# Optimization experiments

Measured on AMD Instinct MI355X. Metric: run time of the kernel, lower is better.

Reference implementation:

```python
import jax, jax.numpy as jnp
import numpy as np

DIM = 512
N_HEADS = 8
N_KV_HEADS = 4
HEAD_DIM = DIM // N_HEADS  # 64
N_REP = N_HEADS // N_KV_HEADS  # 2
THETA = 10000.0
EPS_RMS = 1e-6
EPS_Z = 1e-6


def setup_inputs() -> dict:
    key = jax.random.key(0)
    ks = jax.random.split(key, 6)
    s = 1.0 / np.sqrt(DIM)
    return {
        "x": jax.random.normal(ks[0], (4, 8192, DIM), dtype=jnp.float32),
        "norm_w": jnp.ones((DIM,), dtype=jnp.float32),
        "wq": jax.random.normal(ks[1], (DIM, DIM), dtype=jnp.float32) * s,
        "wk": jax.random.normal(ks[2], (N_KV_HEADS * HEAD_DIM, DIM), dtype=jnp.float32) * s,
        "wv": jax.random.normal(ks[3], (N_KV_HEADS * HEAD_DIM, DIM), dtype=jnp.float32) * s,
        "wo": jax.random.normal(ks[4], (DIM, DIM), dtype=jnp.float32) * s,
    }


def _rope_cos_sin(seq_len, head_dim):
    # freqs_cis = polar(1, t * theta^(-2i/d))
    inv = 1.0 / (THETA ** (jnp.arange(0, head_dim, 2, dtype=jnp.float32) / head_dim))
    ang = jnp.arange(seq_len, dtype=jnp.float32)[:, None] * inv[None, :]  # (S, d/2)
    return jnp.cos(ang), jnp.sin(ang)


def _apply_rope(t, cos, sin):
    # t: (B, S, H, d); complex rotation on consecutive pairs
    B, S, H, d = t.shape
    tr = t.reshape(B, S, H, d // 2, 2)
    xr, xi = tr[..., 0], tr[..., 1]
    c = cos[None, :, None, :]  # (1, S, 1, d/2)
    s = sin[None, :, None, :]
    out = jnp.stack([xr * c - xi * s, xr * s + xi * c], axis=-1)
    return out.reshape(B, S, H, d)


def _forward(x, norm_w, wq, wk, wv, wo):
    B, S, _ = x.shape
    # RMSNorm
    x = x * jax.lax.rsqrt(jnp.mean(x * x, axis=-1, keepdims=True) + EPS_RMS) * norm_w
    xq = (x @ wq.T).reshape(B, S, N_HEADS, HEAD_DIM)
    xk = (x @ wk.T).reshape(B, S, N_KV_HEADS, HEAD_DIM)
    xv = (x @ wv.T).reshape(B, S, N_KV_HEADS, HEAD_DIM)
    cos, sin = _rope_cos_sin(S, HEAD_DIM)
    xq = _apply_rope(xq, cos, sin)
    xk = _apply_rope(xk, cos, sin)
    # repeat_kv: (B,S,Hkv,d) -> (B,S,Hkv*n_rep,d)
    keys = jnp.repeat(xk, N_REP, axis=2)
    values = jnp.repeat(xv, N_REP, axis=2)
    # to (B, H, S, d)
    Q = jnp.transpose(xq, (0, 2, 1, 3))
    K = jnp.transpose(keys, (0, 2, 1, 3))
    V = jnp.transpose(values, (0, 2, 1, 3))
    phi = lambda t: jax.nn.elu(t) + 1.0
    Q_lin, K_lin = phi(Q), phi(K)
    # Faithful to source: elementwise product reduced over s -> (B,H,d)
    KV = jnp.einsum('bhsd,bhsd->bhd', K_lin, V)
    K_sum = K_lin.sum(axis=2)  # (B,H,d)
    Z = jnp.einsum('bhsd,bhd->bhs', Q_lin, K_sum)[..., None]  # (B,H,S,1)
    Y = Q_lin * KV[:, :, None, :] / (Z + EPS_Z)  # (B,H,S,d)
    Y = jnp.transpose(Y, (0, 2, 1, 3)).reshape(B, S, N_HEADS * HEAD_DIM)
    return Y @ wo.T


def reference(x, norm_w, wq, wk, wv, wo):
    return _forward(x, norm_w, wq, wk, wv, wo)
```

## Files before the change

kernel.cpp:

```cpp
#include <hip/hip_runtime.h>
#include <cmath>

typedef __attribute__((ext_vector_type(8))) short short8;
typedef __attribute__((ext_vector_type(4))) float floatx4;

#define T_TOK 32768
#define DIMK 512
#define AKT 2097152

__device__ __forceinline__ unsigned short f2bf(float f) {
  union { float f; unsigned int u; } v; v.f = f;
  unsigned int r = (v.u + 0x7fffu + ((v.u >> 16) & 1u)) >> 16;
  return (unsigned short)r;
}
__device__ __forceinline__ float bf2f(unsigned short h) {
  union { unsigned int u; float f; } v; v.u = ((unsigned int)h) << 16;
  return v.f;
}

__device__ __forceinline__ void gload_lds16(const unsigned short* g, unsigned short* ldsbase) {
  __builtin_amdgcn_global_load_lds(
      (const __attribute__((address_space(1))) unsigned int*)g,
      (__attribute__((address_space(3))) unsigned int*)ldsbase, 16, 0, 0);
}

__global__ __launch_bounds__(256) void k_prep(const float* __restrict__ x,
    const float* __restrict__ norm_w, const float* __restrict__ wq,
    const float* __restrict__ wk, const float* __restrict__ wv,
    const float* __restrict__ wo, unsigned short* __restrict__ Wb,
    unsigned short* __restrict__ wob, float2* __restrict__ rope,
    float* __restrict__ KVz, unsigned short* __restrict__ xn) {
  if (blockIdx.x < 2048) {
    int i = blockIdx.x * 256 + threadIdx.x;
    int R = i >> 9, col = i & 511;
    float v;
    if (i < 262144) {
      v = wq[i];
    } else {
      int h = (R - 512) >> 7, rem = (R - 512) & 127;
      if (rem < 64) v = wk[(h * 64 + rem) * 512 + col];
      else          v = wv[(h * 64 + rem - 64) * 512 + col];
    }
    Wb[(col >> 6) * 65536 + R * 64 + (col & 63)] = f2bf(v);
    if (i < 262144) {
      wob[(col >> 6) * 32768 + R * 64 + (col & 63)] = f2bf(wo[i]);
      int s = i >> 5, m = i & 31;
      const double c0 = 0.74989420933245582;
      double c1 = c0 * c0, c2 = c1 * c1, c3 = c2 * c2, c4 = c3 * c3;
      double p = 1.0;
      if (m & 1)  p *= c0;
      if (m & 2)  p *= c1;
      if (m & 4)  p *= c2;
      if (m & 8)  p *= c3;
      if (m & 16) p *= c4;
      double ang = (double)s * p;
      const double TWO_PI = 6.2831853071795864769;
      double q = rint(ang * (1.0 / TWO_PI));
      double r = fma(-q, TWO_PI, ang);
      float rf = (float)r;
      rope[i] = make_float2(cosf(rf), sinf(rf));
    }
    if (i < 2048) KVz[i] = 0.f;
  } else {
    int bid = blockIdx.x - 2048;
    int wave = threadIdx.x >> 6, lane = threadIdx.x & 63;
    size_t t = (size_t)bid * 4 + wave;
    const float4* xr = (const float4*)(x + t * DIMK);
    float4 a = xr[lane * 2];
    float4 b = xr[lane * 2 + 1];
    float ss = a.x * a.x + a.y * a.y + a.z * a.z + a.w * a.w
             + b.x * b.x + b.y * b.y + b.z * b.z + b.w * b.w;
    #pragma unroll
    for (int off = 32; off >= 1; off >>= 1) ss += __shfl_xor(ss, off, 64);
    float scale = rsqrtf(ss * (1.0f / DIMK) + 1e-6f);
    const float4* wr = (const float4*)norm_w;
    float4 w0 = wr[lane * 2], w1 = wr[lane * 2 + 1];
    uint4 o;
    o.x = (unsigned int)f2bf(a.x * scale * w0.x) | ((unsigned int)f2bf(a.y * scale * w0.y) << 16);
    o.y = (unsigned int)f2bf(a.z * scale * w0.z) | ((unsigned int)f2bf(a.w * scale * w0.w) << 16);
    o.z = (unsigned int)f2bf(b.x * scale * w1.x) | ((unsigned int)f2bf(b.y * scale * w1.y) << 16);
    o.w = (unsigned int)f2bf(b.z * scale * w1.z) | ((unsigned int)f2bf(b.w * scale * w1.w) << 16);
    *(uint4*)(xn + (size_t)(lane >> 3) * AKT + t * 64 + (lane & 7) * 8) = o;
  }
}

template <bool BF16_OUT, bool FUSE>
__global__ __launch_bounds__(512, 2) void k_gemm256(const unsigned short* __restrict__ A,
    const unsigned short* __restrict__ Bw, void* __restrict__ Cv, int ldc, int nrows,
    const float2* __restrict__ rope, float* __restrict__ KV, float* __restrict__ Ksum) {
  extern __shared__ __align__(16) unsigned short smem[];
  unsigned short* const AsP = smem;
  unsigned short* const BsP = smem + 32768;

  const int tid = threadIdx.x;
  const int wave = tid >> 6, lane = tid & 63;
  const int r = lane & 15, quad = lane >> 4, r7 = r & 7;
  const int wm = (wave >> 2) * 128, wn = (wave & 3) * 64;

  const int ngy = gridDim.y;
  const int bid = blockIdx.x + gridDim.x * blockIdx.y;
  const int xcd = bid & 7;
  const int j = bid >> 3;
  const int lg = (ngy == 4) ? 2 : 1;
  const int per = (gridDim.x * ngy) >> (3 + lg);
  const int mt = xcd * per + (j >> lg);
  const int nt = j & (ngy - 1);
  const int m0 = mt * 256, n0 = nt * 256;

  const int srow = lane >> 3;
  const int scb = (lane & 7) ^ srow;
  const size_t bkt = (size_t)nrows * 64;
  const unsigned short* const Asrc = A + (size_t)(m0 + wave * 8 + srow) * 64 + scb * 8;
  const unsigned short* const Bsrc = Bw + (size_t)(n0 + wave * 8 + srow) * 64 + scb * 8;
  unsigned short* const Adst = AsP + wave * 8 * 64;
  unsigned short* const Bdst = BsP + wave * 8 * 64;

#define STAGE_A(buf, h, kt) do { \
    gload_lds16(Asrc + (size_t)(kt) * AKT + (h) * 8192, Adst + (buf) * 16384 + ((h) * 128) * 64); \
    gload_lds16(Asrc + (size_t)(kt) * AKT + (h) * 8192 + 4096, Adst + (buf) * 16384 + ((h) * 128 + 64) * 64); \
  } while (0)
#define STAGE_B(buf, h, kt) do { \
    gload_lds16(Bsrc + (size_t)(kt) * bkt + (h) * 8192, Bdst + (buf) * 16384 + ((h) * 128) * 64); \
    gload_lds16(Bsrc + (size_t)(kt) * bkt + (h) * 8192 + 4096, Bdst + (buf) * 16384 + ((h) * 128 + 64) * 64); \
  } while (0)

  short8 af[4][2], b0[2][2], b1[2][2];
  floatx4 acc[8][4];
  #pragma unroll
  for (int i = 0; i < 8; i++)
    #pragma unroll
    for (int jj = 0; jj < 4; jj++)
      acc[i][jj] = (floatx4){0.f, 0.f, 0.f, 0.f};

#define LDA8(buf, ah) do { \
    _Pragma("unroll") for (int ii = 0; ii < 4; ii++) \
      _Pragma("unroll") for (int kk = 0; kk < 2; kk++) \
        af[ii][kk] = *(const short8*)&AsP[(buf) * 16384 + (wm + (ah) * 64 + ii * 16 + r) * 64 + ((kk * 4 + quad) ^ r7) * 8]; \
  } while (0)
#define LDB4(buf, bh, arr) do { \
    _Pragma("unroll") for (int jj = 0; jj < 2; jj++) \
      _Pragma("unroll") for (int kk = 0; kk < 2; kk++) \
        arr[jj][kk] = *(const short8*)&BsP[(buf) * 16384 + (wn + (bh) * 32 + jj * 16 + r) * 64 + ((kk * 4 + quad) ^ r7) * 8]; \
  } while (0)
#define MFMAQ(ah, bh, arr) do { \
    __builtin_amdgcn_s_setprio(1); \
    _Pragma("unroll") for (int ii = 0; ii < 4; ii++) \
      _Pragma("unroll") for (int jj = 0; jj < 2; jj++) \
        _Pragma("unroll") for (int kk = 0; kk < 2; kk++) \
          acc[(ah) * 4 + ii][(bh) * 2 + jj] = __builtin_amdgcn_mfma_f32_16x16x32_bf16( \
              af[ii][kk], arr[jj][kk], acc[(ah) * 4 + ii][(bh) * 2 + jj], 0, 0, 0); \
    __builtin_amdgcn_s_setprio(0); \
  } while (0)
#define BAR() do { asm volatile("" ::: "memory"); __builtin_amdgcn_s_barrier(); asm volatile("" ::: "memory"); } while (0)
#define VMW(n) do { asm volatile("s_waitcnt vmcnt(" #n ")" ::: "memory"); __builtin_amdgcn_sched_barrier(0); } while (0)

  STAGE_A(0, 0, 0); STAGE_B(0, 0, 0); STAGE_A(0, 1, 0); STAGE_B(0, 1, 0);
  STAGE_A(1, 0, 1); STAGE_B(1, 0, 1); STAGE_A(1, 1, 1); STAGE_B(1, 1, 1);
  VMW(8);
  BAR();

  #pragma unroll
  for (int it = 0; it < 3; ++it) {
    const int kt = it * 2;
    LDA8(0, 0); LDB4(0, 0, b0);
    BAR(); MFMAQ(0, 0, b0); BAR();
    LDB4(0, 1, b1);
    BAR(); MFMAQ(0, 1, b1); BAR();
    LDA8(0, 1); STAGE_B(0, 0, kt + 2); STAGE_B(0, 1, kt + 2);
    BAR(); MFMAQ(1, 1, b1); BAR();
    STAGE_A(0, 0, kt + 2); STAGE_A(0, 1, kt + 2);
    BAR(); MFMAQ(1, 0, b0); VMW(8); BAR();
    LDA8(1, 0); LDB4(1, 0, b0);
    BAR(); MFMAQ(0, 0, b0); BAR();
    LDB4(1, 1, b1);
    BAR(); MFMAQ(0, 1, b1); BAR();
    LDA8(1, 1); STAGE_B(1, 0, kt + 3); STAGE_B(1, 1, kt + 3);
    BAR(); MFMAQ(1, 1, b1); BAR();
    STAGE_A(1, 0, kt + 3); STAGE_A(1, 1, kt + 3);
    BAR(); MFMAQ(1, 0, b0); VMW(8); BAR();
  }

  LDA8(0, 0); LDB4(0, 0, b0);
  BAR(); MFMAQ(0, 0, b0); BAR();
  LDB4(0, 1, b1);
  BAR(); MFMAQ(0, 1, b1); BAR();
  LDA8(0, 1);
  BAR(); MFMAQ(1, 1, b1); BAR();
  MFMAQ(1, 0, b0); VMW(0); BAR();
  LDA8(1, 0); LDB4(1, 0, b0);
  BAR(); MFMAQ(0, 0, b0); BAR();
  LDB4(1, 1, b1);
  BAR(); MFMAQ(0, 1, b1); BAR();
  LDA8(1, 1);
  BAR(); MFMAQ(1, 1, b1); BAR();
  MFMAQ(1, 0, b0);

  if (FUSE && n0 >= 512) {
#define VSW(t, d) ((t) * 128 + ((d) & 15) + (((((d) >> 4) + ((t) >> 2)) & 7) << 4))
    const int b = m0 >> 13;
    const int kh = ((n0 - 512) >> 8) * 2 + (wn >> 7);
    const int hvb = (wn >> 7) << 6;
    float* const Vs = (float*)smem;
    __syncthreads();
    if (wn & 64) {
      #pragma unroll
      for (int i = 0; i < 8; i++)
        #pragma unroll
        for (int j2 = 0; j2 < 4; j2++)
          #pragma unroll
          for (int p = 0; p < 4; p++) {
            int t = wm + i * 16 + quad * 4 + p;
            Vs[VSW(t, hvb + j2 * 16 + r)] = acc[i][j2][p];
          }
    }
    __syncthreads();
    if (!(wn & 64)) {
      float kvp[4] = {0.f, 0.f, 0.f, 0.f};
      float ksp[4] = {0.f, 0.f, 0.f, 0.f};
      #pragma unroll
      for (int i = 0; i < 8; i++)
        #pragma unroll
        for (int p = 0; p < 4; p++) {
          int t = wm + i * 16 + quad * 4 + p;
          int pos = (m0 + t) & 8191;
          #pragma unroll
          for (int j2 = 0; j2 < 4; j2++) {
            float v = acc[i][j2][p];
            float vp = __shfl_xor(v, 1, 64);
            int d = j2 * 16 + r;
            float2 cs = rope[pos * 32 + (d >> 1)];
            float rk = (r & 1) ? (vp * cs.y + v * cs.x) : (v * cs.x - vp * cs.y);
            rk = rk > 0.f ? rk + 1.f : __expf(rk);
            kvp[j2] += rk * Vs[VSW(t, hvb + d)];
            ksp[j2] += rk;
          }
        }
      #pragma unroll
      for (int j2 = 0; j2 < 4; j2++) {
        kvp[j2] += __shfl_xor(kvp[j2], 16, 64); kvp[j2] += __shfl_xor(kvp[j2], 32, 64);
        ksp[j2] += __shfl_xor(ksp[j2], 16, 64); ksp[j2] += __shfl_xor(ksp[j2], 32, 64);
      }
      if (lane < 16) {
        int base = (b * 4 + kh) * 64 + r;
        #pragma unroll
        for (int j2 = 0; j2 < 4; j2++) {
          atomicAdd(&KV[base + j2 * 16], kvp[j2]);
          atomicAdd(&Ksum[base + j2 * 16], ksp[j2]);
        }
      }
    }
#undef VSW
  } else {
    #pragma unroll
    for (int i = 0; i < 8; i++)
      #pragma unroll
      for (int j2 = 0; j2 < 4; j2++) {
        int row = m0 + wm + i * 16 + quad * 4;
        int col = n0 + wn + j2 * 16 + r;
        #pragma unroll
        for (int p = 0; p < 4; p++) {
          if constexpr (BF16_OUT) {
            ((unsigned short*)Cv)[(size_t)(row + p) * ldc + col] = f2bf(acc[i][j2][p]);
          } else {
            ((float*)Cv)[(size_t)(row + p) * ldc + col] = acc[i][j2][p];
          }
        }
      }
  }
#undef STAGE_A
#undef STAGE_B
#undef LDA8
#undef LDB4
#undef MFMAQ
#undef BAR
#undef VMW
}

__global__ __launch_bounds__(256) void k_qkern(const unsigned short* __restrict__ qkv,
    const float2* __restrict__ rope, const float* __restrict__ KV,
    const float* __restrict__ Ksum, unsigned short* __restrict__ Yb) {
  const int h = threadIdx.x >> 5;
  const int pr = threadIdx.x & 31;
  for (int t = blockIdx.x; t < T_TOK; t += gridDim.x) {
    int b = t >> 13, pos = t & 8191;
    unsigned int qp = *(const unsigned int*)(qkv + (size_t)t * 512 + h * 64 + 2 * pr);
    float qx = bf2f((unsigned short)(qp & 0xffffu));
    float qy = bf2f((unsigned short)(qp >> 16));
    float2 cs = rope[pos * 32 + pr];
    float ar = qx * cs.x - qy * cs.y;
    float ai = qx * cs.y + qy * cs.x;
    ar = ar > 0.f ? ar + 1.f : __expf(ar);
    ai = ai > 0.f ? ai + 1.f : __expf(ai);
    int bk = b * 4 + (h >> 1);
    float2 ks = *(const float2*)(Ksum + bk * 64 + 2 * pr);
    float z = ar * ks.x + ai * ks.y;
    #pragma unroll
    for (int off = 16; off >= 1; off >>= 1) z += __shfl_xor(z, off, 64);
    float2 kv = *(const float2*)(KV + bk * 64 + 2 * pr);
    float inv = 1.0f / (z + 1e-6f);
    unsigned int o = (unsigned int)f2bf(ar * kv.x * inv)
                   | ((unsigned int)f2bf(ai * kv.y * inv) << 16);
    *(unsigned int*)(Yb + (size_t)h * AKT + t * 64 + 2 * pr) = o;
  }
}

extern "C" void kernel_launch(void* const* d_in, const int* in_sizes, int n_in,
                              void* d_out, int out_size, void* d_ws, size_t ws_size,
                              hipStream_t stream) {
  const float* x = (const float*)d_in[0];
  const float* norm_w = (const float*)d_in[1];
  const float* wq = (const float*)d_in[2];
  const float* wk = (const float*)d_in[3];
  const float* wv = (const float*)d_in[4];
  const float* wo = (const float*)d_in[5];
  float* out = (float*)d_out;

  char* ws = (char*)d_ws;
  unsigned short* xn  = (unsigned short*)(ws);
  unsigned short* Wb  = (unsigned short*)(ws + 33554432);
  unsigned short* wob = (unsigned short*)(ws + 34603008);
  unsigned short* qkv = (unsigned short*)(ws + 35127296);
  float2* rope        = (float2*)(ws + 102236160);
  float* KV           = (float*)(ws + 104333312);
  float* Ksum         = (float*)(ws + 104337408);
  unsigned short* Yb  = (unsigned short*)(ws + 104341504);

  static bool s_attr = false;
  if (!s_attr) {
    (void)hipFuncSetAttribute(reinterpret_cast<const void*>(&k_gemm256<true, true>),
                              hipFuncAttributeMaxDynamicSharedMemorySize, 131072);
    (void)hipFuncSetAttribute(reinterpret_cast<const void*>(&k_gemm256<false, false>),
                              hipFuncAttributeMaxDynamicSharedMemorySize, 131072);
    s_attr = true;
  }

  k_prep<<<10240, 256, 0, stream>>>(x, norm_w, wq, wk, wv, wo, Wb, wob, rope, KV, xn);
  k_gemm256<true, true><<<dim3(128, 4), 512, 131072, stream>>>(
      xn, Wb, (void*)qkv, 512, 1024, rope, KV, Ksum);
  k_qkern<<<4096, 256, 0, stream>>>(qkv, rope, KV, Ksum, Yb);
  k_gemm256<false, false><<<dim3(128, 2), 512, 131072, stream>>>(
      Yb, wob, (void*)out, 512, 512, nullptr, nullptr, nullptr);
}
```

Before: 219.3 us.

## Replace 256x256 pipelined GEMM with simple 128x128 tile GEMM kernel

Replaces the hand-scheduled 256x256 tile GEMM, which used double-buffered LDS staging, interleaved barriers and priority hints, with a simpler 128x128 tile kernel. The new kernel has 4 waves, 32KB of static shared memory and a single-buffered K loop that syncs around each stage. More, smaller blocks are launched to raise occupancy and parallelism, and the fused KV/Ksum reduction is adapted to one KV head per tile. The cost is losing the overlap of loads with MFMA and adding more atomics and redundant A/B traffic.

```diff
diff --git a/kernel.cpp b/kernel.cpp
--- a/kernel.cpp
+++ b/kernel.cpp
@@ -85,140 +85,89 @@
 }
 
 template <bool BF16_OUT, bool FUSE>
-__global__ __launch_bounds__(512, 2) void k_gemm256(const unsigned short* __restrict__ A,
-    const unsigned short* __restrict__ Bw, void* __restrict__ Cv, int ldc, int nrows,
+__global__ __launch_bounds__(256) void k_gemm128(const unsigned short* __restrict__ A,
+    const unsigned short* __restrict__ Bw, void* __restrict__ Cv, int ldc, int nrows, int lgn,
     const float2* __restrict__ rope, float* __restrict__ KV, float* __restrict__ Ksum) {
-  extern __shared__ __align__(16) unsigned short smem[];
-  unsigned short* const AsP = smem;
-  unsigned short* const BsP = smem + 32768;
+  __shared__ __align__(16) unsigned short smem[16384];
+  unsigned short* const As = smem;
+  unsigned short* const Bs = smem + 8192;
 
   const int tid = threadIdx.x;
   const int wave = tid >> 6, lane = tid & 63;
   const int r = lane & 15, quad = lane >> 4, r7 = r & 7;
-  const int wm = (wave >> 2) * 128, wn = (wave & 3) * 64;
+  const int wm = (wave >> 1) * 64, wn = (wave & 1) * 64;
 
   const int ngy = gridDim.y;
   const int bid = blockIdx.x + gridDim.x * blockIdx.y;
   const int xcd = bid & 7;
   const int j = bid >> 3;
-  const int lg = (ngy == 4) ? 2 : 1;
-  const int per = (gridDim.x * ngy) >> (3 + lg);
-  const int mt = xcd * per + (j >> lg);
+  const int mt = xcd * 32 + (j >> lgn);
   const int nt = j & (ngy - 1);
-  const int m0 = mt * 256, n0 = nt * 256;
+  const int m0 = mt * 128, n0 = nt * 128;
 
   const int srow = lane >> 3;
   const int scb = (lane & 7) ^ srow;
   const size_t bkt = (size_t)nrows * 64;
-  const unsigned short* const Asrc = A + (size_t)(m0 + wave * 8 + srow) * 64 + scb * 8;
-  const unsigned short* const Bsrc = Bw + (size_t)(n0 + wave * 8 + srow) * 64 + scb * 8;
-  unsigned short* const Adst = AsP + wave * 8 * 64;
-  unsigned short* const Bdst = BsP + wave * 8 * 64;
-
-#define STAGE_A(buf, h, kt) do { \
-    gload_lds16(Asrc + (size_t)(kt) * AKT + (h) * 8192, Adst + (buf) * 16384 + ((h) * 128) * 64); \
-    gload_lds16(Asrc + (size_t)(kt) * AKT + (h) * 8192 + 4096, Adst + (buf) * 16384 + ((h) * 128 + 64) * 64); \
-  } while (0)
-#define STAGE_B(buf, h, kt) do { \
-    gload_lds16(Bsrc + (size_t)(kt) * bkt + (h) * 8192, Bdst + (buf) * 16384 + ((h) * 128) * 64); \
-    gload_lds16(Bsrc + (size_t)(kt) * bkt + (h) * 8192 + 4096, Bdst + (buf) * 16384 + ((h) * 128 + 64) * 64); \
-  } while (0)
-
-  short8 af[4][2], b0[2][2], b1[2][2];
-  floatx4 acc[8][4];
+  const unsigned short* const Ag = A  + (size_t)(m0 + wave * 32 + srow) * 64 + scb * 8;
+  const unsigned short* const Bg = Bw + (size_t)(n0 + wave * 32 + srow) * 64 + scb * 8;
+  unsigned short* const Al = As + wave * 32 * 64;
+  unsigned short* const Bl = Bs + wave * 32 * 64;
+
+  floatx4 acc[4][4];
   #pragma unroll
-  for (int i = 0; i < 8; i++)
+  for (int i = 0; i < 4; i++)
     #pragma unroll
     for (int jj = 0; jj < 4; jj++)
       acc[i][jj] = (floatx4){0.f, 0.f, 0.f, 0.f};
 
-#define LDA8(buf, ah) do { \
-    _Pragma("unroll") for (int ii = 0; ii < 4; ii++) \
-      _Pragma("unroll") for (int kk = 0; kk < 2; kk++) \
-        af[ii][kk] = *(const short8*)&AsP[(buf) * 16384 + (wm + (ah) * 64 + ii * 16 + r) * 64 + ((kk * 4 + quad) ^ r7) * 8]; \
-  } while (0)
-#define LDB4(buf, bh, arr) do { \
-    _Pragma("unroll") for (int jj = 0; jj < 2; jj++) \
-      _Pragma("unroll") for (int kk = 0; kk < 2; kk++) \
-        arr[jj][kk] = *(const short8*)&BsP[(buf) * 16384 + (wn + (bh) * 32 + jj * 16 + r) * 64 + ((kk * 4 + quad) ^ r7) * 8]; \
-  } while (0)
-#define MFMAQ(ah, bh, arr) do { \
-    __builtin_amdgcn_s_setprio(1); \
-    _Pragma("unroll") for (int ii = 0; ii < 4; ii++) \
-      _Pragma("unroll") for (int jj = 0; jj < 2; jj++) \
-        _Pragma("unroll") for (int kk = 0; kk < 2; kk++) \
-          acc[(ah) * 4 + ii][(bh) * 2 + jj] = __builtin_amdgcn_mfma_f32_16x16x32_bf16( \
-              af[ii][kk], arr[jj][kk], acc[(ah) * 4 + ii][(bh) * 2 + jj], 0, 0, 0); \
-    __builtin_amdgcn_s_setprio(0); \
-  } while (0)
-#define BAR() do { asm volatile("" ::: "memory"); __builtin_amdgcn_s_barrier(); asm volatile("" ::: "memory"); } while (0)
-#define VMW(n) do { asm volatile("s_waitcnt vmcnt(" #n ")" ::: "memory"); __builtin_amdgcn_sched_barrier(0); } while (0)
-
-  STAGE_A(0, 0, 0); STAGE_B(0, 0, 0); STAGE_A(0, 1, 0); STAGE_B(0, 1, 0);
-  STAGE_A(1, 0, 1); STAGE_B(1, 0, 1); STAGE_A(1, 1, 1); STAGE_B(1, 1, 1);
-  VMW(8);
-  BAR();
-
-  #pragma unroll
-  for (int it = 0; it < 3; ++it) {
-    const int kt = it * 2;
-    LDA8(0, 0); LDB4(0, 0, b0);
-    BAR(); MFMAQ(0, 0, b0); BAR();
-    LDB4(0, 1, b1);
-    BAR(); MFMAQ(0, 1, b1); BAR();
-    LDA8(0, 1); STAGE_B(0, 0, kt + 2); STAGE_B(0, 1, kt + 2);
-    BAR(); MFMAQ(1, 1, b1); BAR();
-    STAGE_A(0, 0, kt + 2); STAGE_A(0, 1, kt + 2);
-    BAR(); MFMAQ(1, 0, b0); VMW(8); BAR();
-    LDA8(1, 0); LDB4(1, 0, b0);
-    BAR(); MFMAQ(0, 0, b0); BAR();
-    LDB4(1, 1, b1);
-    BAR(); MFMAQ(0, 1, b1); BAR();
-    LDA8(1, 1); STAGE_B(1, 0, kt + 3); STAGE_B(1, 1, kt + 3);
-    BAR(); MFMAQ(1, 1, b1); BAR();
-    STAGE_A(1, 0, kt + 3); STAGE_A(1, 1, kt + 3);
-    BAR(); MFMAQ(1, 0, b0); VMW(8); BAR();
-  }
-
-  LDA8(0, 0); LDB4(0, 0, b0);
-  BAR(); MFMAQ(0, 0, b0); BAR();
-  LDB4(0, 1, b1);
-  BAR(); MFMAQ(0, 1, b1); BAR();
-  LDA8(0, 1);
-  BAR(); MFMAQ(1, 1, b1); BAR();
-  MFMAQ(1, 0, b0); VMW(0); BAR();
-  LDA8(1, 0); LDB4(1, 0, b0);
-  BAR(); MFMAQ(0, 0, b0); BAR();
-  LDB4(1, 1, b1);
-  BAR(); MFMAQ(0, 1, b1); BAR();
-  LDA8(1, 1);
-  BAR(); MFMAQ(1, 1, b1); BAR();
-  MFMAQ(1, 0, b0);
+  for (int kt = 0; kt < 8; kt++) {
+    #pragma unroll
+    for (int li = 0; li < 4; li++) {
+      gload_lds16(Ag + (size_t)kt * AKT + li * 512, Al + li * 512);
+      gload_lds16(Bg + (size_t)kt * bkt + li * 512, Bl + li * 512);
+    }
+    __syncthreads();
+    #pragma unroll
+    for (int kk = 0; kk < 64; kk += 32) {
+      const int sw = ((((kk >> 3) + quad)) ^ r7) * 8;
+      short8 af[4], bfv[4];
+      #pragma unroll
+      for (int i = 0; i < 4; i++)
+        af[i] = *(const short8*)&As[(wm + i * 16 + r) * 64 + sw];
+      #pragma unroll
+      for (int jj = 0; jj < 4; jj++)
+        bfv[jj] = *(const short8*)&Bs[(wn + jj * 16 + r) * 64 + sw];
+      #pragma unroll
+      for (int i = 0; i < 4; i++)
+        #pragma unroll
+        for (int jj = 0; jj < 4; jj++)
+          acc[i][jj] = __builtin_amdgcn_mfma_f32_16x16x32_bf16(af[i], bfv[jj], acc[i][jj], 0, 0, 0);
+    }
+    __syncthreads();
+  }
 
   if (FUSE && n0 >= 512) {
-#define VSW(t, d) ((t) * 128 + ((d) & 15) + (((((d) >> 4) + ((t) >> 2)) & 7) << 4))
+#define VSW(t, d) ((t) * 64 + ((d) & 15) + (((((d) >> 4) + ((t) >> 2)) & 3) << 4))
     const int b = m0 >> 13;
-    const int kh = ((n0 - 512) >> 8) * 2 + (wn >> 7);
-    const int hvb = (wn >> 7) << 6;
+    const int kh = (n0 - 512) >> 7;
     float* const Vs = (float*)smem;
-    __syncthreads();
-    if (wn & 64) {
-      #pragma unroll
-      for (int i = 0; i < 8; i++)
+    if (wn) {
+      #pragma unroll
+      for (int i = 0; i < 4; i++)
         #pragma unroll
         for (int j2 = 0; j2 < 4; j2++)
           #pragma unroll
           for (int p = 0; p < 4; p++) {
             int t = wm + i * 16 + quad * 4 + p;
-            Vs[VSW(t, hvb + j2 * 16 + r)] = acc[i][j2][p];
+            Vs[VSW(t, j2 * 16 + r)] = acc[i][j2][p];
           }
     }
     __syncthreads();
-    if (!(wn & 64)) {
+    if (!wn) {
       float kvp[4] = {0.f, 0.f, 0.f, 0.f};
       float ksp[4] = {0.f, 0.f, 0.f, 0.f};
       #pragma unroll
-      for (int i = 0; i < 8; i++)
+      for (int i = 0; i < 4; i++)
         #pragma unroll
         for (int p = 0; p < 4; p++) {
           int t = wm + i * 16 + quad * 4 + p;
@@ -231,7 +180,7 @@
             float2 cs = rope[pos * 32 + (d >> 1)];
             float rk = (r & 1) ? (vp * cs.y + v * cs.x) : (v * cs.x - vp * cs.y);
             rk = rk > 0.f ? rk + 1.f : __expf(rk);
-            kvp[j2] += rk * Vs[VSW(t, hvb + d)];
+            kvp[j2] += rk * Vs[VSW(t, d)];
             ksp[j2] += rk;
           }
         }
@@ -252,7 +201,7 @@
 #undef VSW
   } else {
     #pragma unroll
-    for (int i = 0; i < 8; i++)
+    for (int i = 0; i < 4; i++)
       #pragma unroll
       for (int j2 = 0; j2 < 4; j2++) {
         int row = m0 + wm + i * 16 + quad * 4;
@@ -267,13 +216,6 @@
         }
       }
   }
-#undef STAGE_A
-#undef STAGE_B
-#undef LDA8
-#undef LDB4
-#undef MFMAQ
-#undef BAR
-#undef VMW
 }
 
 __global__ __launch_bounds__(256) void k_qkern(const unsigned short* __restrict__ qkv,
@@ -325,19 +267,10 @@
   float* Ksum         = (float*)(ws + 104337408);
   unsigned short* Yb  = (unsigned short*)(ws + 104341504);
 
-  static bool s_attr = false;
-  if (!s_attr) {
-    (void)hipFuncSetAttribute(reinterpret_cast<const void*>(&k_gemm256<true, true>),
-                              hipFuncAttributeMaxDynamicSharedMemorySize, 131072);
-    (void)hipFuncSetAttribute(reinterpret_cast<const void*>(&k_gemm256<false, false>),
-                              hipFuncAttributeMaxDynamicSharedMemorySize, 131072);
-    s_attr = true;
-  }
-
   k_prep<<<10240, 256, 0, stream>>>(x, norm_w, wq, wk, wv, wo, Wb, wob, rope, KV, xn);
-  k_gemm256<true, true><<<dim3(128, 4), 512, 131072, stream>>>(
-      xn, Wb, (void*)qkv, 512, 1024, rope, KV, Ksum);
+  k_gemm128<true, true><<<dim3(256, 8), 256, 0, stream>>>(
+      xn, Wb, (void*)qkv, 512, 1024, 3, rope, KV, Ksum);
   k_qkern<<<4096, 256, 0, stream>>>(qkv, rope, KV, Ksum, Yb);
-  k_gemm256<false, false><<<dim3(128, 2), 512, 131072, stream>>>(
-      Yb, wob, (void*)out, 512, 512, nullptr, nullptr, nullptr);
-}
+  k_gemm128<false, false><<<dim3(256, 4), 256, 0, stream>>>(
+      Yb, wob, (void*)out, 512, 512, 2, nullptr, nullptr, nullptr);
+}
```

Result: slower. 229.5 us (+4.6%).
